# Optimization experiments

Measured on AMD Instinct MI355X. Metric: run time of the kernel, lower is better.

Reference implementation:

```python
import jax, jax.numpy as jnp
import numpy as np
import math

B, C, A, W, H = 8, 128, 16, 64, 64


def setup_inputs() -> dict:
    key = jax.random.key(0)
    ks = jax.random.split(key, 7)
    s_in = 1.0 / math.sqrt(C)
    return {
        "x": jax.random.normal(ks[0], (B, C, W, H), dtype=jnp.float32),
        "Wq": jax.random.normal(ks[1], (A, C), dtype=jnp.float32) * s_in,
        "bq": jnp.zeros((A,), dtype=jnp.float32),
        "Wk": jax.random.normal(ks[2], (A, C), dtype=jnp.float32) * s_in,
        "bk": jnp.zeros((A,), dtype=jnp.float32),
        "Wv": jax.random.normal(ks[3], (C, C), dtype=jnp.float32) * s_in,
        "bv": jnp.zeros((C,), dtype=jnp.float32),
    }


def reference(x, Wq, bq, Wk, bk, Wv, bv):
    # 1x1 convs == per-pixel linear projections
    q = jnp.einsum('ac,bcwh->bawh', Wq, x) + bq[None, :, None, None]  # [B,A,W,H]
    k = jnp.einsum('ac,bcwh->bawh', Wk, x) + bk[None, :, None, None]  # [B,A,W,H]
    v = jnp.einsum('vc,bcwh->bvwh', Wv, x) + bv[None, :, None, None]  # [B,C,W,H]

    scale = 1.0 / math.sqrt(q.shape[1])
    # full spatial attention: [B, W, H, W, H]
    attn = jnp.einsum('bawh,baWH->bwhWH', q, k)
    b, w, h, _, _ = attn.shape
    attn = jax.nn.softmax(attn.reshape(b, w, h, -1) * scale, axis=-1)
    attn = attn.reshape(b, w, h, w, h)
    out = jnp.einsum('bwhWH,bvWH->bvwh', attn, v)  # [B,C,W,H]
    return out
```

## Files before the change

### kernel.cpp

```cpp
#include <hip/hip_runtime.h>
#include <math.h>

#define BB 8
#define CC 128
#define NN 4096

typedef _Float16 f16;
typedef _Float16 f16x4v __attribute__((ext_vector_type(4)));
typedef _Float16 f16x8 __attribute__((ext_vector_type(8)));
typedef float f32x16 __attribute__((ext_vector_type(16)));

#if __has_builtin(__builtin_amdgcn_exp2f)
#define EXP2(x) __builtin_amdgcn_exp2f(x)
#else
#define EXP2(x) __expf((x)*0.69314718056f)
#endif

#define QSCALE 0.360673760222f
#define SHIFT  5.770780163555f

#define WF_BYTES 65536

__global__ __launch_bounds__(256)
void prep_kernel(const float* __restrict__ Wq, const float* __restrict__ bq,
                 const float* __restrict__ Wk, const float* __restrict__ bk,
                 const float* __restrict__ Wv, const float* __restrict__ bv,
                 f16* __restrict__ Wf, float* __restrict__ biasS)
{
    const int tg = blockIdx.x*256 + threadIdx.x;
    if (tg < 2560) {
        const int mt = tg >> 9, ks = (tg >> 6) & 7, l = tg & 63;
        const int n32 = l & 31, h = l >> 5;
        const int r = mt*32 + n32;
        f16x8 v8;
        #pragma unroll
        for (int i = 0; i < 8; i++) {
            int c = ks*16 + 8*h + i;
            float wv_;
            if (r < 16)      wv_ = QSCALE * Wq[r*CC + c];
            else if (r < 32) wv_ = Wk[(r-16)*CC + c];
            else             wv_ = Wv[(r-32)*CC + c];
            v8[i] = (f16)wv_;
        }
        *(f16x8*)&Wf[(size_t)tg*8] = v8;
    }
    if (blockIdx.x == 0 && threadIdx.x < 160) {
        int r = threadIdx.x;
        biasS[r] = r < 16 ? QSCALE*bq[r] : (r < 32 ? bk[r-16] : bv[r-32]);
    }
}

__global__ __launch_bounds__(256)
void proj_kernel(const float* __restrict__ x, const f16* __restrict__ Wf,
                 const float* __restrict__ biasS,
                 f16* __restrict__ Qt, f16* __restrict__ Kt, f16* __restrict__ Vf)
{
    __shared__ __align__(16) f16 Vl[CC*140];

    const int tid  = threadIdx.x;
    const int lane = tid & 63;
    const int wv   = tid >> 6;
    const int b    = blockIdx.x & 7;
    const int pt   = blockIdx.x >> 3;
    const int n32  = lane & 31;
    const int half = lane >> 5;
    const int p    = pt*128 + wv*32 + n32;

    const float* xp = x + (size_t)b*CC*NN + p;
    f16x8 xf[8];
    #pragma unroll
    for (int ks = 0; ks < 8; ks++) {
        float xv[8];
        #pragma unroll
        for (int i = 0; i < 8; i++)
            xv[i] = __builtin_nontemporal_load(&xp[(size_t)(ks*16 + 8*half + i)*NN]);
        #pragma unroll
        for (int i = 0; i < 8; i++) xf[ks][i] = (f16)xv[i];
    }

    f32x16 acc[5];
    #pragma unroll
    for (int mt = 0; mt < 5; mt++) acc[mt] = (f32x16)0.0f;
    #pragma unroll
    for (int ks = 0; ks < 8; ks++) {
        #pragma unroll
        for (int mt = 0; mt < 5; mt++) {
            f16x8 wfr = *(const f16x8*)&Wf[((size_t)(mt*8 + ks)*64 + lane)*8];
            acc[mt] = __builtin_amdgcn_mfma_f32_32x32x16_f16(wfr, xf[ks], acc[mt], 0, 0, 0);
        }
    }

    #pragma unroll
    for (int mt = 0; mt < 5; mt++) {
        #pragma unroll
        for (int q = 0; q < 4; q++) {
            float4 b4 = *(const float4*)&biasS[mt*32 + q*8 + 4*half];
            acc[mt][q*4+0] += b4.x; acc[mt][q*4+1] += b4.y;
            acc[mt][q*4+2] += b4.z; acc[mt][q*4+3] += b4.w;
        }
    }

    {
        size_t qkoff = ((size_t)b*NN + p)*16;
        f16x4v s0, s1, s2, s3;
        #pragma unroll
        for (int i = 0; i < 4; i++) {
            s0[i] = (f16)acc[0][i];    s1[i] = (f16)acc[0][4+i];
            s2[i] = (f16)acc[0][8+i];  s3[i] = (f16)acc[0][12+i];
        }
        *(f16x4v*)&Qt[qkoff + 4*half]     = s0;
        *(f16x4v*)&Qt[qkoff + 8 + 4*half] = s1;
        *(f16x4v*)&Kt[qkoff + 4*half]     = s2;
        *(f16x4v*)&Kt[qkoff + 8 + 4*half] = s3;
    }

    #pragma unroll
    for (int mt = 1; mt < 5; mt++) {
        #pragma unroll
        for (int g = 0; g < 16; g++) {
            int c = (mt-1)*32 + (g & 3) + 8*(g >> 2) + 4*half;
            Vl[c*140 + wv*32 + n32] = (f16)acc[mt][g];
        }
    }
    __syncthreads();

    #pragma unroll
    for (int pass = 0; pass < 8; pass++) {
        int item = pass*256 + tid;
        int l    = item & 63;
        int f    = (item >> 6) & 15;
        int ktl  = item >> 10;
        int kc   = f >> 2, ct = f & 3;
        int li   = l & 31, h2 = l >> 5;
        const f16* src = &Vl[(ct*32 + li)*140 + ktl*64 + kc*16 + 4*h2];
        f16x4v lo = *(const f16x4v*)&src[0];
        f16x4v hi = *(const f16x4v*)&src[8];
        f16x8 v8;
        #pragma unroll
        for (int i = 0; i < 4; i++) { v8[i] = lo[i]; v8[4+i] = hi[i]; }
        int ktg = pt*2 + ktl;
        *(f16x8*)&Vf[((((size_t)b*64 + ktg)*16 + f)*64 + l)*8] = v8;
    }
}

__global__ __launch_bounds__(256, 2)
void attn_kernel(const f16* __restrict__ Qt, const f16* __restrict__ Kt,
                 const f16* __restrict__ Vf, float* __restrict__ out)
{
    __shared__ __align__(16) unsigned char lds_raw[27776];

    const int tid  = threadIdx.x;
    const int lane = tid & 63;
    const int wv   = tid >> 6;
    const int b    = blockIdx.x & 7;
    const int qt   = blockIdx.x >> 3;
    const int q0   = qt*32;
    const int n32  = lane & 31;
    const int half = lane >> 5;

    const f16* vb = Vf + (size_t)b*64*16*512;
    const f16* kb = Kt + (size_t)b*NN*16;
    const f16x8 qf = *(const f16x8*)&Qt[((size_t)b*NN + q0 + n32)*16 + half*8];

    f32x16 of[4];
    #pragma unroll
    for (int ct = 0; ct < 4; ct++) of[ct] = (f32x16)0.0f;
    float ps[4] = {0.f, 0.f, 0.f, 0.f};

    f16x8 kf0 = *(const f16x8*)&kb[((size_t)wv*64 + n32)*16 + half*8];
    f16x8 kf1 = *(const f16x8*)&kb[((size_t)wv*64 + 32 + n32)*16 + half*8];
    f16x8 vpf[16];
    {
        const f16* vt = vb + (size_t)wv*8192;
        #pragma unroll
        for (int i = 0; i < 16; i++)
            vpf[i] = *(const f16x8*)&vt[((size_t)i*64 + lane)*8];
    }

    for (int kt = wv; kt < NN/64; kt += 4) {
        const int ktn = (kt + 4 < NN/64) ? kt + 4 : kt;
        f16x8 kf0n = *(const f16x8*)&kb[((size_t)ktn*64 + n32)*16 + half*8];
        f16x8 kf1n = *(const f16x8*)&kb[((size_t)ktn*64 + 32 + n32)*16 + half*8];

        f32x16 St0 = __builtin_amdgcn_mfma_f32_32x32x16_f16(kf0, qf, (f32x16)(-SHIFT), 0, 0, 0);
        f32x16 St1 = __builtin_amdgcn_mfma_f32_32x32x16_f16(kf1, qf, (f32x16)(-SHIFT), 0, 0, 0);

        f16x8 pf[4];
        #pragma unroll
        for (int g = 0; g < 16; g++) {
            float e0 = EXP2(St0[g]); ps[g & 3] += e0; pf[(g >> 3)][g & 7]     = (f16)e0;
            float e1 = EXP2(St1[g]); ps[g & 3] += e1; pf[2 + (g >> 3)][g & 7] = (f16)e1;
        }

        const f16* vtn = vb + (size_t)ktn*8192;
        #pragma unroll
        for (int kc = 0; kc < 4; kc++) {
            #pragma unroll
            for (int ct = 0; ct < 4; ct++) {
                const int i = kc*4 + ct;
                f16x8 vc = vpf[i];
                vpf[i] = *(const f16x8*)&vtn[((size_t)i*64 + lane)*8];
                of[ct] = __builtin_amdgcn_mfma_f32_32x32x16_f16(pf[kc], vc, of[ct], 0, 0, 0);
            }
        }
        kf0 = kf0n; kf1 = kf1n;
    }

    float ls = (ps[0] + ps[1]) + (ps[2] + ps[3]);
    ls += __shfl_xor(ls, 32);

    __syncthreads();
    if (wv != 0) {
        unsigned char* base = lds_raw + (size_t)(wv-1)*9216 + (size_t)lane*144;
        #pragma unroll
        for (int ct = 0; ct < 4; ct++) {
            #pragma unroll
            for (int h = 0; h < 2; h++) {
                f16x8 t;
                #pragma unroll
                for (int jj = 0; jj < 8; jj++) t[jj] = (f16)of[ct][h*8+jj];
                *(f16x8*)(base + ct*32 + h*16) = t;
            }
        }
        *(float*)(base + 128) = ls;
    }
    __syncthreads();
    if (wv == 0) {
        #pragma unroll
        for (int s2 = 0; s2 < 3; s2++) {
            unsigned char* base = lds_raw + (size_t)s2*9216 + (size_t)lane*144;
            #pragma unroll
            for (int ct = 0; ct < 4; ct++) {
                #pragma unroll
                for (int h = 0; h < 2; h++) {
                    f16x8 t = *(const f16x8*)(base + ct*32 + h*16);
                    #pragma unroll
                    for (int jj = 0; jj < 8; jj++) of[ct][h*8+jj] += (float)t[jj];
                }
            }
            ls += *(const float*)(base + 128);
        }
        float* ls_inv = (float*)(lds_raw + 27648);
        if (lane < 32) ls_inv[lane] = 1.f / ls;
        float invq[16];
        #pragma unroll
        for (int g = 0; g < 16; g++)
            invq[g] = ls_inv[(g & 3) + 8*(g >> 2) + 4*half];
        float* Tb = (float*)lds_raw;
        #pragma unroll
        for (int ct = 0; ct < 4; ct++) {
            #pragma unroll
            for (int g = 0; g < 16; g++) {
                int row = (g & 3) + 8*(g >> 2) + 4*half;
                Tb[(ct*32 + n32)*36 + row] = of[ct][g] * invq[g];
            }
        }
    }
    __syncthreads();
    {
        const float* Tb = (const float*)lds_raw;
        #pragma unroll
        for (int it = 0; it < 4; it++) {
            int idx = it*256 + tid;
            int c = idx >> 3, qq = idx & 7;
            *(float4*)&out[((size_t)b*CC + c)*NN + q0 + qq*4] =
                *(const float4*)&Tb[c*36 + qq*4];
        }
    }
}

extern "C" void kernel_launch(void* const* d_in, const int* in_sizes, int n_in,
                              void* d_out, int out_size, void* d_ws, size_t ws_size,
                              hipStream_t stream) {
    const float* x  = (const float*)d_in[0];
    const float* Wq = (const float*)d_in[1];
    const float* bq = (const float*)d_in[2];
    const float* Wk = (const float*)d_in[3];
    const float* bk = (const float*)d_in[4];
    const float* Wv = (const float*)d_in[5];
    const float* bv = (const float*)d_in[6];
    float* out = (float*)d_out;

    f16* Qw = (f16*)d_ws;
    f16* Kw = Qw + (size_t)BB*NN*16;
    f16* Vw = Kw + (size_t)BB*NN*16;
    unsigned char* tail = (unsigned char*)d_out + (size_t)out_size*4 - WF_BYTES;
    f16*   Wf    = (f16*)tail;
    float* biasS = (float*)(tail + 49152);

    hipLaunchKernelGGL(prep_kernel, dim3(10), dim3(256), 0, stream,
                       Wq, bq, Wk, bk, Wv, bv, Wf, biasS);
    hipLaunchKernelGGL(proj_kernel, dim3(256), dim3(256), 0, stream,
                       x, Wf, biasS, Qw, Kw, Vw);
    hipLaunchKernelGGL(attn_kernel, dim3(1024), dim3(256), 0, stream,
                       Qw, Kw, Vw, out);
}
```

Measured before the change: 138.8 us.

## Share V tiles across two query groups via async LDS staging in attention

The attention kernel now handles 64 queries per block, split across two wave pairs. Each pair covers half of the key range in 32-key steps. V tiles are double-buffered in LDS through global_load_lds, so they are loaded once per block and shared by the waves instead of being read from global memory by every wave into registers. The proj kernel writes V in a new 32-key fragment layout to match. This halves the grid, doubles LDS use and adds a block barrier on every iteration, which may reduce occupancy and latency hiding.

```diff
diff --git a/kernel.cpp b/kernel.cpp
--- a/kernel.cpp
+++ b/kernel.cpp
@@ -20,6 +20,12 @@
 #define SHIFT  5.770780163555f
 
 #define WF_BYTES 65536
+
+__device__ __forceinline__ void stage16(const f16* g, f16* l) {
+    __builtin_amdgcn_global_load_lds(
+        (const __attribute__((address_space(1))) unsigned int*)g,
+        (__attribute__((address_space(3))) unsigned int*)l, 16, 0, 0);
+}
 
 __global__ __launch_bounds__(256)
 void prep_kernel(const float* __restrict__ Wq, const float* __restrict__ bq,
@@ -130,16 +136,17 @@
         int l    = item & 63;
         int f    = (item >> 6) & 15;
         int ktl  = item >> 10;
-        int kc   = f >> 2, ct = f & 3;
+        int c16  = f >> 2, ct = f & 3;
         int li   = l & 31, h2 = l >> 5;
-        const f16* src = &Vl[(ct*32 + li)*140 + ktl*64 + kc*16 + 4*h2];
+        const f16* src = &Vl[(ct*32 + li)*140 + ktl*64 + c16*16 + 4*h2];
         f16x4v lo = *(const f16x4v*)&src[0];
         f16x4v hi = *(const f16x4v*)&src[8];
         f16x8 v8;
         #pragma unroll
         for (int i = 0; i < 4; i++) { v8[i] = lo[i]; v8[4+i] = hi[i]; }
-        int ktg = pt*2 + ktl;
-        *(f16x8*)&Vf[((((size_t)b*64 + ktg)*16 + f)*64 + l)*8] = v8;
+        int kt32 = (pt*2 + ktl)*2 + (c16 >> 1);
+        int frag = (c16 & 1)*4 + ct;
+        *(f16x8*)&Vf[(((size_t)b*128 + kt32)*8 + frag)*512 + (size_t)l*8] = v8;
     }
 }
 
@@ -147,18 +154,22 @@
 void attn_kernel(const f16* __restrict__ Qt, const f16* __restrict__ Kt,
                  const f16* __restrict__ Vf, float* __restrict__ out)
 {
-    __shared__ __align__(16) unsigned char lds_raw[27776];
+    __shared__ __align__(16) unsigned char lds_raw[51456];
 
     const int tid  = threadIdx.x;
     const int lane = tid & 63;
     const int wv   = tid >> 6;
+    const int wvu  = __builtin_amdgcn_readfirstlane(wv);
+    const int qsub = wv & 1;
+    const int kpar = wv >> 1;
     const int b    = blockIdx.x & 7;
-    const int qt   = blockIdx.x >> 3;
-    const int q0   = qt*32;
+    const int qg   = blockIdx.x >> 3;
+    const int q0   = qg*64 + qsub*32;
     const int n32  = lane & 31;
     const int half = lane >> 5;
 
-    const f16* vb = Vf + (size_t)b*64*16*512;
+    f16* Vbuf = (f16*)lds_raw;
+    const f16* vb = Vf + (size_t)b*128*4096;
     const f16* kb = Kt + (size_t)b*NN*16;
     const f16x8 qf = *(const f16x8*)&Qt[((size_t)b*NN + q0 + n32)*16 + half*8];
 
@@ -167,92 +178,94 @@
     for (int ct = 0; ct < 4; ct++) of[ct] = (f32x16)0.0f;
     float ps[4] = {0.f, 0.f, 0.f, 0.f};
 
-    f16x8 kf0 = *(const f16x8*)&kb[((size_t)wv*64 + n32)*16 + half*8];
-    f16x8 kf1 = *(const f16x8*)&kb[((size_t)wv*64 + 32 + n32)*16 + half*8];
-    f16x8 vpf[16];
-    {
-        const f16* vt = vb + (size_t)wv*8192;
-        #pragma unroll
-        for (int i = 0; i < 16; i++)
-            vpf[i] = *(const f16x8*)&vt[((size_t)i*64 + lane)*8];
-    }
-
-    for (int kt = wv; kt < NN/64; kt += 4) {
-        const int ktn = (kt + 4 < NN/64) ? kt + 4 : kt;
-        f16x8 kf0n = *(const f16x8*)&kb[((size_t)ktn*64 + n32)*16 + half*8];
-        f16x8 kf1n = *(const f16x8*)&kb[((size_t)ktn*64 + 32 + n32)*16 + half*8];
-
-        f32x16 St0 = __builtin_amdgcn_mfma_f32_32x32x16_f16(kf0, qf, (f32x16)(-SHIFT), 0, 0, 0);
-        f32x16 St1 = __builtin_amdgcn_mfma_f32_32x32x16_f16(kf1, qf, (f32x16)(-SHIFT), 0, 0, 0);
-
-        f16x8 pf[4];
-        #pragma unroll
-        for (int g = 0; g < 16; g++) {
-            float e0 = EXP2(St0[g]); ps[g & 3] += e0; pf[(g >> 3)][g & 7]     = (f16)e0;
-            float e1 = EXP2(St1[g]); ps[g & 3] += e1; pf[2 + (g >> 3)][g & 7] = (f16)e1;
-        }
-
-        const f16* vtn = vb + (size_t)ktn*8192;
-        #pragma unroll
-        for (int kc = 0; kc < 4; kc++) {
-            #pragma unroll
-            for (int ct = 0; ct < 4; ct++) {
-                const int i = kc*4 + ct;
-                f16x8 vc = vpf[i];
-                vpf[i] = *(const f16x8*)&vtn[((size_t)i*64 + lane)*8];
-                of[ct] = __builtin_amdgcn_mfma_f32_32x32x16_f16(pf[kc], vc, of[ct], 0, 0, 0);
-            }
-        }
-        kf0 = kf0n; kf1 = kf1n;
+    #define DO_STAGE(nb, ii)                                                    \
+        {                                                                       \
+            _Pragma("unroll")                                                   \
+            for (int p_ = 0; p_ < 4; p_++) {                                    \
+                int seg_ = wvu*4 + p_;                                          \
+                int kp_ = seg_ >> 3, fr_ = seg_ & 7;                            \
+                int ktv_ = 2*(ii) + kp_;                                        \
+                stage16(vb + ((size_t)ktv_*8 + fr_)*512 + (size_t)lane*8,       \
+                        Vbuf + (size_t)(nb)*8192 + kp_*4096 + fr_*512);         \
+            }                                                                   \
+        }
+
+    f16x8 kf = *(const f16x8*)&kb[((size_t)(kpar*32) + n32)*16 + half*8];
+    DO_STAGE(0, 0);
+    __syncthreads();
+
+    for (int i = 0; i < 64; i++) {
+        const int cb = i & 1, nb = cb ^ 1;
+        if (i + 1 < 64) DO_STAGE(nb, i + 1);
+        const int ktn = (i + 1 < 64) ? (2*(i+1) + kpar) : (2*i + kpar);
+        f16x8 kfn = *(const f16x8*)&kb[((size_t)ktn*32 + n32)*16 + half*8];
+
+        f32x16 St = __builtin_amdgcn_mfma_f32_32x32x16_f16(kf, qf, (f32x16)(-SHIFT), 0, 0, 0);
+
+        f16x8 pf0, pf1;
+        #pragma unroll
+        for (int g = 0; g < 8; g++) {
+            float e0 = EXP2(St[g]);     ps[g & 3] += e0; pf0[g] = (f16)e0;
+            float e1 = EXP2(St[8 + g]); ps[g & 3] += e1; pf1[g] = (f16)e1;
+        }
+
+        const f16* vt = Vbuf + (size_t)cb*8192 + kpar*4096;
+        #pragma unroll
+        for (int ct = 0; ct < 4; ct++) {
+            f16x8 v0 = *(const f16x8*)&vt[(size_t)ct*512 + (size_t)lane*8];
+            of[ct] = __builtin_amdgcn_mfma_f32_32x32x16_f16(pf0, v0, of[ct], 0, 0, 0);
+            f16x8 v1 = *(const f16x8*)&vt[(size_t)(4 + ct)*512 + (size_t)lane*8];
+            of[ct] = __builtin_amdgcn_mfma_f32_32x32x16_f16(pf1, v1, of[ct], 0, 0, 0);
+        }
+        kf = kfn;
+        __syncthreads();
     }
 
     float ls = (ps[0] + ps[1]) + (ps[2] + ps[3]);
     ls += __shfl_xor(ls, 32);
 
-    __syncthreads();
-    if (wv != 0) {
-        unsigned char* base = lds_raw + (size_t)(wv-1)*9216 + (size_t)lane*144;
+    if (kpar == 1) {
+        unsigned char* base = lds_raw + 32768 + (size_t)(qsub*64 + lane)*144;
         #pragma unroll
         for (int ct = 0; ct < 4; ct++) {
             #pragma unroll
             for (int h = 0; h < 2; h++) {
                 f16x8 t;
                 #pragma unroll
-                for (int jj = 0; jj < 8; jj++) t[jj] = (f16)of[ct][h*8+jj];
+                for (int j = 0; j < 8; j++) t[j] = (f16)of[ct][h*8+j];
                 *(f16x8*)(base + ct*32 + h*16) = t;
             }
         }
         *(float*)(base + 128) = ls;
     }
     __syncthreads();
-    if (wv == 0) {
-        #pragma unroll
-        for (int s2 = 0; s2 < 3; s2++) {
-            unsigned char* base = lds_raw + (size_t)s2*9216 + (size_t)lane*144;
+    if (kpar == 0) {
+        unsigned char* base = lds_raw + 32768 + (size_t)(qsub*64 + lane)*144;
+        #pragma unroll
+        for (int ct = 0; ct < 4; ct++) {
             #pragma unroll
-            for (int ct = 0; ct < 4; ct++) {
+            for (int h = 0; h < 2; h++) {
+                f16x8 t = *(const f16x8*)(base + ct*32 + h*16);
                 #pragma unroll
-                for (int h = 0; h < 2; h++) {
-                    f16x8 t = *(const f16x8*)(base + ct*32 + h*16);
-                    #pragma unroll
-                    for (int jj = 0; jj < 8; jj++) of[ct][h*8+jj] += (float)t[jj];
-                }
+                for (int j = 0; j < 8; j++) of[ct][h*8+j] += (float)t[j];
             }
-            ls += *(const float*)(base + 128);
-        }
-        float* ls_inv = (float*)(lds_raw + 27648);
-        if (lane < 32) ls_inv[lane] = 1.f / ls;
+        }
+        ls += *(const float*)(base + 128);
+
+        float* ls_inv = (float*)(lds_raw + 51200);
+        if (lane < 32) ls_inv[qsub*32 + lane] = 1.f / ls;
         float invq[16];
         #pragma unroll
         for (int g = 0; g < 16; g++)
-            invq[g] = ls_inv[(g & 3) + 8*(g >> 2) + 4*half];
+            invq[g] = ls_inv[qsub*32 + (g & 3) + 8*(g >> 2) + 4*half];
+
         float* Tb = (float*)lds_raw;
         #pragma unroll
         for (int ct = 0; ct < 4; ct++) {
             #pragma unroll
             for (int g = 0; g < 16; g++) {
                 int row = (g & 3) + 8*(g >> 2) + 4*half;
-                Tb[(ct*32 + n32)*36 + row] = of[ct][g] * invq[g];
+                Tb[(ct*32 + n32)*68 + qsub*32 + row] = of[ct][g] * invq[g];
             }
         }
     }
@@ -260,11 +273,11 @@
     {
         const float* Tb = (const float*)lds_raw;
         #pragma unroll
-        for (int it = 0; it < 4; it++) {
+        for (int it = 0; it < 8; it++) {
             int idx = it*256 + tid;
-            int c = idx >> 3, qq = idx & 7;
-            *(float4*)&out[((size_t)b*CC + c)*NN + q0 + qq*4] =
-                *(const float4*)&Tb[c*36 + qq*4];
+            int c = idx >> 4, q4 = idx & 15;
+            *(float4*)&out[((size_t)b*CC + c)*NN + qg*64 + q4*4] =
+                *(const float4*)&Tb[c*68 + q4*4];
         }
     }
 }
@@ -292,6 +305,6 @@
                        Wq, bq, Wk, bk, Wv, bv, Wf, biasS);
     hipLaunchKernelGGL(proj_kernel, dim3(256), dim3(256), 0, stream,
                        x, Wf, biasS, Qw, Kw, Vw);
-    hipLaunchKernelGGL(attn_kernel, dim3(1024), dim3(256), 0, stream,
+    hipLaunchKernelGGL(attn_kernel, dim3(512), dim3(256), 0, stream,
                        Qw, Kw, Vw, out);
 }
```

New measurement: 138.7 us. No clear change (-0.1%).
